# Kernel optimization log

Measured on AMD Instinct MI355X. Metric: run time of the kernel, lower is better.

Reference implementation:

```python
import jax, jax.numpy as jnp
import numpy as np

N = 8192
C_IN = 128
C_OUT = 128


def setup_inputs() -> dict:
    key = jax.random.key(0)
    k1, k2, k3, k4 = jax.random.split(key, 4)
    x = jax.random.normal(k1, (N, C_IN), dtype=jnp.float32)
    adj = jax.random.uniform(k2, (N, N), dtype=jnp.float32)
    mask = jax.random.uniform(k3, (N, N), dtype=jnp.float32)
    # nn.Linear(c_in, c_out, bias=False) weight has shape [c_out, c_in]
    W = jax.random.normal(k4, (C_OUT, C_IN), dtype=jnp.float32) * (1.0 / np.sqrt(C_IN))
    return {"x": x, "adj": adj, "mask": mask, "W": W}


def reference(x, adj, mask, W):
    n = adj.shape[0]
    # adj = adj * mask + I  (mask application plus self-loops)
    adj_eff = adj * mask + jnp.eye(n, dtype=adj.dtype)
    # h = x @ W^T  (Linear, no bias), then aggregate: out = adj_eff @ h
    h = jnp.einsum("nc,oc->no", x, W)  # [N, c_out]
    return jnp.matmul(adj_eff, h)       # [N, c_out]
```

## Files before the change

kernel.cpp:

```cpp
#include <hip/hip_runtime.h>
#include <hip/hip_bf16.h>
#include <stdint.h>

#define NROW 8192
#define CD 128
#define SPLITK 8
#define KCHUNK (NROW / SPLITK)
#define KSTEPS (KCHUNK / 32)

typedef __bf16 bf16_t;
typedef __bf16 bf16x8 __attribute__((ext_vector_type(8)));
typedef float f32x4 __attribute__((ext_vector_type(4)));

__device__ __forceinline__ f32x4 mfma16(bf16x8 a, bf16x8 b, f32x4 c) {
    return __builtin_amdgcn_mfma_f32_16x16x32_bf16(a, b, c, 0, 0, 0);
}

__device__ __forceinline__ bf16x8 load_cvt_bf16(const float* __restrict__ p) {
    f32x4 a0 = *(const f32x4*)p;
    f32x4 a1 = *(const f32x4*)(p + 4);
    bf16x8 r;
    r[0] = (bf16_t)a0.x; r[1] = (bf16_t)a0.y; r[2] = (bf16_t)a0.z; r[3] = (bf16_t)a0.w;
    r[4] = (bf16_t)a1.x; r[5] = (bf16_t)a1.y; r[6] = (bf16_t)a1.z; r[7] = (bf16_t)a1.w;
    return r;
}

__global__ __launch_bounds__(64)
void h_kernel(const float* __restrict__ x, const float* __restrict__ W,
              bf16_t* __restrict__ hT, float* __restrict__ out)
{
    __shared__ __align__(16) float hs[16 * 128];
    const int lane = threadIdx.x;
    const int m = lane & 15, q = lane >> 4;
    const int rb = blockIdx.x * 16;

    f32x4 acc[8] = {};
#pragma unroll
    for (int k0 = 0; k0 < CD; k0 += 32) {
        bf16x8 af = load_cvt_bf16(x + (size_t)(rb + m) * CD + k0 + q * 8);
#pragma unroll
        for (int c = 0; c < 8; ++c) {
            bf16x8 bv = load_cvt_bf16(W + (size_t)(c * 16 + m) * CD + k0 + q * 8);
            acc[c] = mfma16(af, bv, acc[c]);
        }
    }
#pragma unroll
    for (int c = 0; c < 8; ++c)
#pragma unroll
        for (int j = 0; j < 4; ++j)
            hs[(q * 4 + j) * 128 + c * 16 + m] = acc[c][j];
    __syncthreads();

    float* dst = out + (size_t)rb * CD;
#pragma unroll
    for (int t = 0; t < 8; ++t) {
        int fi = t * 64 + lane;
        *(f32x4*)(dst + fi * 4) = *(const f32x4*)(hs + fi * 4);
    }
#pragma unroll
    for (int t = 0; t < 4; ++t) {
        int idx = t * 64 + lane;
        int c = idx >> 1, nc = idx & 1;
        bf16x8 v;
#pragma unroll
        for (int j = 0; j < 8; ++j)
            v[j] = (bf16_t)hs[(nc * 8 + j) * 128 + c];
        *(bf16x8*)(hT + (size_t)c * NROW + rb + nc * 8) = v;
    }
}

template <bool ATOMIC>
__global__ __launch_bounds__(256)
void gemm_kernel(const float* __restrict__ adj, const float* __restrict__ mask,
                 const bf16_t* __restrict__ hT, float* __restrict__ outp)
{
    const int tid  = threadIdx.x;
    const int w    = tid >> 6;
    const int lane = tid & 63;
    const int m = lane & 15, q = lane >> 4;
    const int row  = blockIdx.x * 64 + w * 16 + m;
    const int kbeg = blockIdx.y * KCHUNK;

    const float*  pa = adj  + (size_t)row * NROW + kbeg + q * 8;
    const float*  pm = mask + (size_t)row * NROW + kbeg + q * 8;
    const bf16_t* pb = hT   + (size_t)m   * NROW + kbeg + q * 8;

    f32x4 acc[8] = {};

    f32x4 aA0, aA1, xA0, xA1, aB0, aB1, xB0, xB1;
    bf16x8 bA[8], bB[8];

    auto loadA = [&](int it, f32x4& a0, f32x4& a1, f32x4& x0, f32x4& x1) {
        const float* p0 = pa + it * 32;
        const float* p1 = pm + it * 32;
        a0 = __builtin_nontemporal_load((const f32x4*)p0);
        a1 = __builtin_nontemporal_load((const f32x4*)(p0 + 4));
        x0 = __builtin_nontemporal_load((const f32x4*)p1);
        x1 = __builtin_nontemporal_load((const f32x4*)(p1 + 4));
    };
    auto loadB = [&](int it, bf16x8* b) {
#pragma unroll
        for (int c = 0; c < 8; ++c)
            b[c] = *(const bf16x8*)(pb + (size_t)c * 16 * NROW + it * 32);
    };
    auto comp = [&](const f32x4& a0, const f32x4& a1,
                    const f32x4& x0, const f32x4& x1, const bf16x8* b) {
        bf16x8 af;
        af[0] = (bf16_t)(a0.x * x0.x);
        af[1] = (bf16_t)(a0.y * x0.y);
        af[2] = (bf16_t)(a0.z * x0.z);
        af[3] = (bf16_t)(a0.w * x0.w);
        af[4] = (bf16_t)(a1.x * x1.x);
        af[5] = (bf16_t)(a1.y * x1.y);
        af[6] = (bf16_t)(a1.z * x1.z);
        af[7] = (bf16_t)(a1.w * x1.w);
#pragma unroll
        for (int c = 0; c < 8; ++c)
            acc[c] = mfma16(af, b[c], acc[c]);
    };

    loadA(0, aA0, aA1, xA0, xA1);
    loadB(0, bA);
#pragma unroll
    for (int it = 0; it < KSTEPS / 2; ++it) {
        loadA(2 * it + 1, aB0, aB1, xB0, xB1);
        loadB(2 * it + 1, bB);
        comp(aA0, aA1, xA0, xA1, bA);
        if (it + 1 < KSTEPS / 2) {
            loadA(2 * it + 2, aA0, aA1, xA0, xA1);
            loadB(2 * it + 2, bA);
        }
        comp(aB0, aB1, xB0, xB1, bB);
    }

    if (!ATOMIC) {
        float* dst = outp + (size_t)blockIdx.y * ((size_t)NROW * CD)
                   + (size_t)(blockIdx.x * 64 + w * 16) * CD;
#pragma unroll
        for (int c = 0; c < 8; ++c)
#pragma unroll
            for (int j = 0; j < 4; ++j)
                __builtin_nontemporal_store(acc[c][j],
                    dst + (q * 4 + j) * CD + c * 16 + m);
    } else {
        float* dst = outp + (size_t)(blockIdx.x * 64 + w * 16) * CD;
#pragma unroll
        for (int c = 0; c < 8; ++c)
#pragma unroll
            for (int j = 0; j < 4; ++j)
                atomicAdd(dst + (q * 4 + j) * CD + c * 16 + m, acc[c][j]);
    }
}

__global__ void reduce_kernel(float* __restrict__ out, const float* __restrict__ part)
{
    const size_t i = ((size_t)blockIdx.x * 256 + threadIdx.x) * 4;
    f32x4 sum = *(const f32x4*)(out + i);
#pragma unroll
    for (int sp = 0; sp < SPLITK; ++sp) {
        f32x4 p = __builtin_nontemporal_load(
            (const f32x4*)(part + (size_t)sp * ((size_t)NROW * CD) + i));
        sum += p;
    }
    *(f32x4*)(out + i) = sum;
}

extern "C" void kernel_launch(void* const* d_in, const int* in_sizes, int n_in,
                              void* d_out, int out_size, void* d_ws, size_t ws_size,
                              hipStream_t stream)
{
    const float* x    = (const float*)d_in[0];
    const float* adj  = (const float*)d_in[1];
    const float* mask = (const float*)d_in[2];
    const float* W    = (const float*)d_in[3];
    float* out = (float*)d_out;

    bf16_t* hT = (bf16_t*)d_ws;
    const size_t HT_BYTES   = (size_t)CD * NROW * sizeof(bf16_t);
    const size_t PART_BYTES = (size_t)SPLITK * NROW * CD * sizeof(float);

    h_kernel<<<dim3(NROW / 16), dim3(64), 0, stream>>>(x, W, hT, out);

    if (ws_size >= HT_BYTES + PART_BYTES) {
        float* part = (float*)((char*)d_ws + HT_BYTES);
        gemm_kernel<false><<<dim3(NROW / 64, SPLITK), dim3(256), 0, stream>>>(adj, mask, hT, part);
        reduce_kernel<<<dim3(1024), dim3(256), 0, stream>>>(out, part);
    } else {
        gemm_kernel<true><<<dim3(NROW / 64, SPLITK), dim3(256), 0, stream>>>(adj, mask, hT, out);
    }
}
```

Before: 699.4 us.

## Stage masked adjacency through swizzled LDS with row-coalesced loads and fewer splits

The main GEMM now has each wave load whole rows of adj and mask as contiguous 1KB spans. It forms the bf16 product and writes it into a double-buffered, XOR-swizzled LDS tile, then reads MFMA fragments back from LDS. The old per-lane strided 32-byte fragment loads are gone. Split-K drops from 8 to 4, which shrinks the partial-sum traffic. h_kernel is batched to 4 waves per block, and nontemporal hints are removed. In exchange the GEMM uses 64KB of LDS and needs a block barrier every 256-wide round, which may limit occupancy.

```diff
diff --git a/kernel.cpp b/kernel.cpp
--- a/kernel.cpp
+++ b/kernel.cpp
@@ -4,12 +4,14 @@
 
 #define NROW 8192
 #define CD 128
-#define SPLITK 8
+#define SPLITK 4
 #define KCHUNK (NROW / SPLITK)
-#define KSTEPS (KCHUNK / 32)
+#define BK2 256
+#define ROUNDS (KCHUNK / BK2)
 
 typedef __bf16 bf16_t;
 typedef __bf16 bf16x8 __attribute__((ext_vector_type(8)));
+typedef __bf16 bf16x4 __attribute__((ext_vector_type(4)));
 typedef float f32x4 __attribute__((ext_vector_type(4)));
 
 __device__ __forceinline__ f32x4 mfma16(bf16x8 a, bf16x8 b, f32x4 c) {
@@ -25,14 +27,15 @@
     return r;
 }
 
-__global__ __launch_bounds__(64)
+__global__ __launch_bounds__(256)
 void h_kernel(const float* __restrict__ x, const float* __restrict__ W,
               bf16_t* __restrict__ hT, float* __restrict__ out)
 {
-    __shared__ __align__(16) float hs[16 * 128];
-    const int lane = threadIdx.x;
+    __shared__ __align__(16) float h_sl_all[4][16 * 128];
+    const int tid = threadIdx.x;
+    const int w = tid >> 6, lane = tid & 63;
     const int m = lane & 15, q = lane >> 4;
-    const int rb = blockIdx.x * 16;
+    const int rb = blockIdx.x * 64 + w * 16;
 
     f32x4 acc[8] = {};
 #pragma unroll
@@ -44,12 +47,12 @@
             acc[c] = mfma16(af, bv, acc[c]);
         }
     }
+    float* hs = h_sl_all[w];
 #pragma unroll
     for (int c = 0; c < 8; ++c)
 #pragma unroll
         for (int j = 0; j < 4; ++j)
             hs[(q * 4 + j) * 128 + c * 16 + m] = acc[c][j];
-    __syncthreads();
 
     float* dst = out + (size_t)rb * CD;
 #pragma unroll
@@ -70,80 +73,90 @@
 }
 
 template <bool ATOMIC>
-__global__ __launch_bounds__(256)
+__global__ __launch_bounds__(256, 2)
 void gemm_kernel(const float* __restrict__ adj, const float* __restrict__ mask,
                  const bf16_t* __restrict__ hT, float* __restrict__ outp)
 {
+    __shared__ __align__(16) ushort prod[2][64 * 256];
+
     const int tid  = threadIdx.x;
     const int w    = tid >> 6;
     const int lane = tid & 63;
     const int m = lane & 15, q = lane >> 4;
-    const int row  = blockIdx.x * 64 + w * 16 + m;
+    const int rowbase = blockIdx.x * 64;
     const int kbeg = blockIdx.y * KCHUNK;
 
-    const float*  pa = adj  + (size_t)row * NROW + kbeg + q * 8;
-    const float*  pm = mask + (size_t)row * NROW + kbeg + q * 8;
-    const bf16_t* pb = hT   + (size_t)m   * NROW + kbeg + q * 8;
+    const bf16_t* pb = hT + (size_t)m * NROW + kbeg + q * 8;
 
     f32x4 acc[8] = {};
-
-    f32x4 aA0, aA1, xA0, xA1, aB0, aB1, xB0, xB1;
-    bf16x8 bA[8], bB[8];
-
-    auto loadA = [&](int it, f32x4& a0, f32x4& a1, f32x4& x0, f32x4& x1) {
-        const float* p0 = pa + it * 32;
-        const float* p1 = pm + it * 32;
-        a0 = __builtin_nontemporal_load((const f32x4*)p0);
-        a1 = __builtin_nontemporal_load((const f32x4*)(p0 + 4));
-        x0 = __builtin_nontemporal_load((const f32x4*)p1);
-        x1 = __builtin_nontemporal_load((const f32x4*)(p1 + 4));
+    f32x4 vaA[8], vxA[8], vaB[8], vxB[8];
+
+    auto issueG = [&](int it, int g, f32x4* va, f32x4* vx) {
+        const int kw = kbeg + it * BK2;
+#pragma unroll
+        for (int rr = 0; rr < 8; ++rr) {
+            int row = w * 16 + g * 8 + rr;
+            const float* pA = adj  + (size_t)(rowbase + row) * NROW + kw + lane * 4;
+            const float* pM = mask + (size_t)(rowbase + row) * NROW + kw + lane * 4;
+            va[rr] = *(const f32x4*)pA;
+            vx[rr] = *(const f32x4*)pM;
+        }
     };
-    auto loadB = [&](int it, bf16x8* b) {
-#pragma unroll
-        for (int c = 0; c < 8; ++c)
-            b[c] = *(const bf16x8*)(pb + (size_t)c * 16 * NROW + it * 32);
+    auto processG = [&](int g, ushort* buf, const f32x4* va, const f32x4* vx) {
+#pragma unroll
+        for (int rr = 0; rr < 8; ++rr) {
+            int row = w * 16 + g * 8 + rr;
+            bf16x4 p;
+            p[0] = (bf16_t)(va[rr].x * vx[rr].x);
+            p[1] = (bf16_t)(va[rr].y * vx[rr].y);
+            p[2] = (bf16_t)(va[rr].z * vx[rr].z);
+            p[3] = (bf16_t)(va[rr].w * vx[rr].w);
+            *(bf16x4*)(buf + row * 256 + (((lane >> 1) ^ (row & 7)) << 3)
+                       + (lane & 1) * 4) = p;
+        }
     };
-    auto comp = [&](const f32x4& a0, const f32x4& a1,
-                    const f32x4& x0, const f32x4& x1, const bf16x8* b) {
-        bf16x8 af;
-        af[0] = (bf16_t)(a0.x * x0.x);
-        af[1] = (bf16_t)(a0.y * x0.y);
-        af[2] = (bf16_t)(a0.z * x0.z);
-        af[3] = (bf16_t)(a0.w * x0.w);
-        af[4] = (bf16_t)(a1.x * x1.x);
-        af[5] = (bf16_t)(a1.y * x1.y);
-        af[6] = (bf16_t)(a1.z * x1.z);
-        af[7] = (bf16_t)(a1.w * x1.w);
-#pragma unroll
-        for (int c = 0; c < 8; ++c)
-            acc[c] = mfma16(af, b[c], acc[c]);
+    auto computeH = [&](const ushort* buf, int it, int h) {
+#pragma unroll
+        for (int s = 0; s < 4; ++s) {
+            int ks = h * 4 + s;
+            bf16x8 af = *(const bf16x8*)(buf + (w * 16 + m) * 256
+                                         + (((ks * 4 + q) ^ (m & 7)) << 3));
+#pragma unroll
+            for (int c = 0; c < 8; ++c) {
+                bf16x8 bv = *(const bf16x8*)(pb + (size_t)c * 16 * NROW
+                                             + it * BK2 + ks * 32);
+                acc[c] = mfma16(af, bv, acc[c]);
+            }
+        }
     };
 
-    loadA(0, aA0, aA1, xA0, xA1);
-    loadB(0, bA);
-#pragma unroll
-    for (int it = 0; it < KSTEPS / 2; ++it) {
-        loadA(2 * it + 1, aB0, aB1, xB0, xB1);
-        loadB(2 * it + 1, bB);
-        comp(aA0, aA1, xA0, xA1, bA);
-        if (it + 1 < KSTEPS / 2) {
-            loadA(2 * it + 2, aA0, aA1, xA0, xA1);
-            loadB(2 * it + 2, bA);
-        }
-        comp(aB0, aB1, xB0, xB1, bB);
+    issueG(0, 0, vaA, vxA);
+    processG(0, (ushort*)prod[0], vaA, vxA);
+    issueG(0, 1, vaB, vxB);
+    processG(1, (ushort*)prod[0], vaB, vxB);
+
+    for (int it = 0; it < ROUNDS; ++it) {
+        __syncthreads();
+        const bool nx = it + 1 < ROUNDS;
+        const ushort* cur = prod[it & 1];
+        ushort* nxt = (ushort*)prod[(it + 1) & 1];
+        if (nx) issueG(it + 1, 0, vaA, vxA);
+        computeH(cur, it, 0);
+        if (nx) { processG(0, nxt, vaA, vxA); issueG(it + 1, 1, vaB, vxB); }
+        computeH(cur, it, 1);
+        if (nx) processG(1, nxt, vaB, vxB);
     }
 
     if (!ATOMIC) {
         float* dst = outp + (size_t)blockIdx.y * ((size_t)NROW * CD)
-                   + (size_t)(blockIdx.x * 64 + w * 16) * CD;
+                   + (size_t)(rowbase + w * 16) * CD;
 #pragma unroll
         for (int c = 0; c < 8; ++c)
 #pragma unroll
             for (int j = 0; j < 4; ++j)
-                __builtin_nontemporal_store(acc[c][j],
-                    dst + (q * 4 + j) * CD + c * 16 + m);
+                dst[(q * 4 + j) * CD + c * 16 + m] = acc[c][j];
     } else {
-        float* dst = outp + (size_t)(blockIdx.x * 64 + w * 16) * CD;
+        float* dst = outp + (size_t)(rowbase + w * 16) * CD;
 #pragma unroll
         for (int c = 0; c < 8; ++c)
 #pragma unroll
@@ -158,8 +171,7 @@
     f32x4 sum = *(const f32x4*)(out + i);
 #pragma unroll
     for (int sp = 0; sp < SPLITK; ++sp) {
-        f32x4 p = __builtin_nontemporal_load(
-            (const f32x4*)(part + (size_t)sp * ((size_t)NROW * CD) + i));
+        f32x4 p = *(const f32x4*)(part + (size_t)sp * ((size_t)NROW * CD) + i);
         sum += p;
     }
     *(f32x4*)(out + i) = sum;
@@ -179,7 +191,7 @@
     const size_t HT_BYTES   = (size_t)CD * NROW * sizeof(bf16_t);
     const size_t PART_BYTES = (size_t)SPLITK * NROW * CD * sizeof(float);
 
-    h_kernel<<<dim3(NROW / 16), dim3(64), 0, stream>>>(x, W, hT, out);
+    h_kernel<<<dim3(NROW / 64), dim3(256), 0, stream>>>(x, W, hT, out);
 
     if (ws_size >= HT_BYTES + PART_BYTES) {
         float* part = (float*)((char*)d_ws + HT_BYTES);
```

Measured after the change: 636.8 us. 9.0% less time.
